# Performance work log

Hardware: AMD Instinct MI355X
Metric: run time of the kernel (lower is better)

## Reference

```python
import jax, jax.numpy as jnp
import numpy as np
from math import sqrt

BLOCK = 64  # block_size from init_kwargs


def setup_inputs() -> dict:
    key = jax.random.key(0)
    kq, kk, kv = jax.random.split(key, 3)
    b, t, e = 16, 8192, 64
    return {
        "Q": jax.random.normal(kq, (b, t, e), dtype=jnp.float32),
        "K": jax.random.normal(kk, (b, t, e), dtype=jnp.float32),
        "V": jax.random.normal(kv, (b, t, e), dtype=jnp.float32),
    }


def reference(Q, K, V):
    b, t, e = Q.shape
    # strided column indices: last position of every block
    cols = jnp.arange(BLOCK - 1, t, BLOCK)            # [n_cols] = [t // BLOCK]
    # scores of every query against the gathered key columns
    Z = jnp.einsum('bte,bce->btc', Q, K[:, cols]) / sqrt(e)  # [b, t, n_cols]
    # causal mask: query at position i may not attend to a column j > i
    causal = jnp.arange(t)[:, None] < cols[None, :]   # [t, n_cols], True = masked
    Z = jnp.where(causal, -jnp.inf, Z)
    # rows before the first column (i < BLOCK-1) are fully masked -> keep zeros
    A = jnp.zeros_like(Z).at[:, BLOCK - 1:].set(
        jax.nn.softmax(Z[:, BLOCK - 1:], axis=-1))
    out = jnp.einsum('btc,bce->bte', A, V[:, cols])   # [b, t, e]
    return out, A
```

## Files before the change

kernel.cpp:

```cpp
#include <hip/hip_runtime.h>
#include <math.h>


#define TSEQ 8192
#define EDIM 64
#define NCOL 128
#define NBATCH 16
#define MPG 4

typedef __attribute__((ext_vector_type(8))) short short8;
typedef __attribute__((ext_vector_type(4))) short short4v;
typedef __attribute__((ext_vector_type(4))) float f32x4;

__device__ __forceinline__ unsigned short f2bf(float f) {
    unsigned int u = __float_as_uint(f);
    return (unsigned short)((u + 0x7fffu + ((u >> 16) & 1u)) >> 16);
}

__global__ __launch_bounds__(256, 2)
void cba_kernel(const float* __restrict__ Q,
                const float* __restrict__ K,
                const float* __restrict__ V,
                float* __restrict__ Out,
                float* __restrict__ A)
{
    __shared__ unsigned short Kc[NCOL][72];
    __shared__ unsigned short VcT[EDIM][136];
    __shared__ unsigned short Aw[64][136];

    const int tid  = threadIdx.x;
    const int lane = tid & 63;
    const int wid  = tid >> 6;
    const int b    = blockIdx.x >> 5;
    const int mg   = blockIdx.x & 31;

    const int c   = lane & 15;
    const int g   = lane >> 4;
    const int kq  = g << 3;
    const int cb  = g << 2;
    const int r   = (wid << 4) + c;

    float4 qf[4];
    {
        const int m0 = mg * MPG;
        const float* qp = Q + ((size_t)b * TSEQ + (m0 << 6) + r) * EDIM;
        qf[0] = *(const float4*)(qp + kq);
        qf[1] = *(const float4*)(qp + kq + 4);
        qf[2] = *(const float4*)(qp + 32 + kq);
        qf[3] = *(const float4*)(qp + 32 + kq + 4);
    }

    {
        const int j = tid >> 1;
        const int h = (tid & 1) << 5;
        const size_t src = ((size_t)b * TSEQ + (j * 64 + 63)) * EDIM + h;
        const float4* ks = (const float4*)(K + src);
        const float4* vs = (const float4*)(V + src);
        #pragma unroll
        for (int t = 0; t < 8; ++t) {
            float4 kf = ks[t];
            unsigned int p0 = (unsigned int)f2bf(kf.x) | ((unsigned int)f2bf(kf.y) << 16);
            unsigned int p1 = (unsigned int)f2bf(kf.z) | ((unsigned int)f2bf(kf.w) << 16);
            *(unsigned int*)&Kc[j][h + 4 * t]     = p0;
            *(unsigned int*)&Kc[j][h + 4 * t + 2] = p1;
        }
        #pragma unroll
        for (int t = 0; t < 8; ++t) {
            float4 vf = vs[t];
            VcT[h + 4 * t + 0][j] = f2bf(vf.x);
            VcT[h + 4 * t + 1][j] = f2bf(vf.y);
            VcT[h + 4 * t + 2][j] = f2bf(vf.z);
            VcT[h + 4 * t + 3][j] = f2bf(vf.w);
        }
    }
    __syncthreads();

    for (int it = 0; it < MPG; ++it) {
        const int m = mg * MPG + it;
        const size_t rowbase = (size_t)b * TSEQ + ((size_t)m << 6);

        short8 qa[2];
        #pragma unroll
        for (int s = 0; s < 2; ++s) {
            float4 f0 = qf[2 * s], f1 = qf[2 * s + 1];
            short8 v;
            v[0] = (short)f2bf(f0.x * 0.125f); v[1] = (short)f2bf(f0.y * 0.125f);
            v[2] = (short)f2bf(f0.z * 0.125f); v[3] = (short)f2bf(f0.w * 0.125f);
            v[4] = (short)f2bf(f1.x * 0.125f); v[5] = (short)f2bf(f1.y * 0.125f);
            v[6] = (short)f2bf(f1.z * 0.125f); v[7] = (short)f2bf(f1.w * 0.125f);
            qa[s] = v;
        }

        f32x4 acc[8];
        #pragma unroll
        for (int t = 0; t < 8; ++t) acc[t] = (f32x4)0.f;
        #pragma unroll
        for (int t = 0; t < 8; ++t) {
            const unsigned short* kr = &Kc[(t << 4) + c][0];
            short8 b0 = *(const short8*)(kr + kq);
            short8 b1 = *(const short8*)(kr + 32 + kq);
            acc[t] = __builtin_amdgcn_mfma_f32_16x16x32_bf16(b0, qa[0], acc[t], 0, 0, 0);
            acc[t] = __builtin_amdgcn_mfma_f32_16x16x32_bf16(b1, qa[1], acc[t], 0, 0, 0);
        }

        if (it + 1 < MPG) {
            const float* qp = Q + (rowbase + 64 + r) * EDIM;
            qf[0] = *(const float4*)(qp + kq);
            qf[1] = *(const float4*)(qp + kq + 4);
            qf[2] = *(const float4*)(qp + 32 + kq);
            qf[3] = *(const float4*)(qp + 32 + kq + 4);
        }

        const int nv = m + (r == 63 ? 1 : 0);
        float sum = 0.f;
        #pragma unroll
        for (int t = 0; t < 8; ++t) {
            const int j0 = (t << 4) + cb;
            #pragma unroll
            for (int reg = 0; reg < 4; ++reg) {
                float e = (j0 + reg < nv) ? __expf(acc[t][reg]) : 0.f;
                acc[t][reg] = e;
                sum += e;
            }
        }
        sum += __shfl_xor(sum, 16);
        sum += __shfl_xor(sum, 32);
        const float rinv = (sum > 0.f) ? 1.0f / sum : 0.f;
        #pragma unroll
        for (int t = 0; t < 8; ++t) {
            acc[t][0] *= rinv; acc[t][1] *= rinv;
            acc[t][2] *= rinv; acc[t][3] *= rinv;
        }

        {
            float* ap = A + (rowbase + r) * NCOL + cb;
            #pragma unroll
            for (int t = 0; t < 8; ++t)
                *(f32x4*)(ap + (t << 4)) = acc[t];
        }

        asm volatile("" ::: "memory");
        #pragma unroll
        for (int t = 0; t < 8; ++t) {
            short4v w;
            w[0] = (short)f2bf(acc[t][0]); w[1] = (short)f2bf(acc[t][1]);
            w[2] = (short)f2bf(acc[t][2]); w[3] = (short)f2bf(acc[t][3]);
            *(short4v*)&Aw[r][(t << 4) + cb] = w;
        }
        asm volatile("s_waitcnt lgkmcnt(0)" ::: "memory");

        short8 af[4];
        {
            const unsigned short* ar = &Aw[r][0];
            #pragma unroll
            for (int s = 0; s < 4; ++s)
                af[s] = *(const short8*)(ar + (s << 5) + kq);
        }
        f32x4 oacc[4];
        #pragma unroll
        for (int te = 0; te < 4; ++te) oacc[te] = (f32x4)0.f;
        #pragma unroll
        for (int te = 0; te < 4; ++te) {
            const unsigned short* vr = &VcT[(te << 4) + c][0];
            #pragma unroll
            for (int s = 0; s < 4; ++s) {
                short8 va = *(const short8*)(vr + (s << 5) + kq);
                oacc[te] = __builtin_amdgcn_mfma_f32_16x16x32_bf16(va, af[s], oacc[te], 0, 0, 0);
            }
        }

        {
            float* op = Out + (rowbase + r) * EDIM + cb;
            #pragma unroll
            for (int te = 0; te < 4; ++te)
                *(f32x4*)(op + (te << 4)) = oacc[te];
        }
    }
}

extern "C" void kernel_launch(void* const* d_in, const int* in_sizes, int n_in,
                              void* d_out, int out_size, void* d_ws, size_t ws_size,
                              hipStream_t stream) {
    const float* Q = (const float*)d_in[0];
    const float* K = (const float*)d_in[1];
    const float* V = (const float*)d_in[2];
    float* Out = (float*)d_out;
    float* A   = Out + (size_t)NBATCH * TSEQ * EDIM;

    cba_kernel<<<dim3(NBATCH * 32), dim3(256), 0, stream>>>(Q, K, V, Out, A);
}
```

Before: 174.8 us.

## Replace LDS staging of attention weights with lane shuffles and double the grid

The softmax weights are now moved from the score accumulator layout into MFMA A-operand layout with cross-lane shuffles instead of a write and read through a shared-memory tile. Dropping that tile frees LDS, which allows 4 blocks per CU instead of 2. Each block now handles 2 row groups instead of 4, so the grid doubles to 1024 blocks. The cost is that the K/V column gather and bf16 conversion into shared memory run twice as often, and the shuffles add instructions of their own.

```diff
diff --git a/kernel.cpp b/kernel.cpp
--- a/kernel.cpp
+++ b/kernel.cpp
@@ -6,18 +6,20 @@
 #define EDIM 64
 #define NCOL 128
 #define NBATCH 16
-#define MPG 4
+#define MPG 2
 
 typedef __attribute__((ext_vector_type(8))) short short8;
-typedef __attribute__((ext_vector_type(4))) short short4v;
 typedef __attribute__((ext_vector_type(4))) float f32x4;
 
 __device__ __forceinline__ unsigned short f2bf(float f) {
     unsigned int u = __float_as_uint(f);
     return (unsigned short)((u + 0x7fffu + ((u >> 16) & 1u)) >> 16);
 }
+__device__ __forceinline__ unsigned int packbf(float a, float b) {
+    return (unsigned int)f2bf(a) | ((unsigned int)f2bf(b) << 16);
+}
 
-__global__ __launch_bounds__(256, 2)
+__global__ __launch_bounds__(256, 4)
 void cba_kernel(const float* __restrict__ Q,
                 const float* __restrict__ K,
                 const float* __restrict__ V,
@@ -26,13 +28,12 @@
 {
     __shared__ unsigned short Kc[NCOL][72];
     __shared__ unsigned short VcT[EDIM][136];
-    __shared__ unsigned short Aw[64][136];
 
     const int tid  = threadIdx.x;
     const int lane = tid & 63;
     const int wid  = tid >> 6;
-    const int b    = blockIdx.x >> 5;
-    const int mg   = blockIdx.x & 31;
+    const int b    = blockIdx.x >> 6;
+    const int mg   = blockIdx.x & 63;
 
     const int c   = lane & 15;
     const int g   = lane >> 4;
@@ -59,10 +60,8 @@
         #pragma unroll
         for (int t = 0; t < 8; ++t) {
             float4 kf = ks[t];
-            unsigned int p0 = (unsigned int)f2bf(kf.x) | ((unsigned int)f2bf(kf.y) << 16);
-            unsigned int p1 = (unsigned int)f2bf(kf.z) | ((unsigned int)f2bf(kf.w) << 16);
-            *(unsigned int*)&Kc[j][h + 4 * t]     = p0;
-            *(unsigned int*)&Kc[j][h + 4 * t + 2] = p1;
+            *(unsigned int*)&Kc[j][h + 4 * t]     = packbf(kf.x, kf.y);
+            *(unsigned int*)&Kc[j][h + 4 * t + 2] = packbf(kf.z, kf.w);
         }
         #pragma unroll
         for (int t = 0; t < 8; ++t) {
@@ -74,6 +73,10 @@
         }
     }
     __syncthreads();
+
+    const int srcA  = c + ((((g << 1)    ) & 3) << 4);
+    const int srcB  = c + ((((g << 1) + 1) & 3) << 4);
+    const bool hiSel = (lane & 32) != 0;
 
     for (int it = 0; it < MPG; ++it) {
         const int m = mg * MPG + it;
@@ -139,23 +142,27 @@
                 *(f32x4*)(ap + (t << 4)) = acc[t];
         }
 
-        asm volatile("" ::: "memory");
+        unsigned int w[16];
         #pragma unroll
         for (int t = 0; t < 8; ++t) {
-            short4v w;
-            w[0] = (short)f2bf(acc[t][0]); w[1] = (short)f2bf(acc[t][1]);
-            w[2] = (short)f2bf(acc[t][2]); w[3] = (short)f2bf(acc[t][3]);
-            *(short4v*)&Aw[r][(t << 4) + cb] = w;
+            w[2 * t]     = packbf(acc[t][0], acc[t][1]);
+            w[2 * t + 1] = packbf(acc[t][2], acc[t][3]);
         }
-        asm volatile("s_waitcnt lgkmcnt(0)" ::: "memory");
 
         short8 af[4];
-        {
-            const unsigned short* ar = &Aw[r][0];
+        #pragma unroll
+        for (int s = 0; s < 4; ++s) {
+            union { unsigned int d[4]; short8 v; } u;
             #pragma unroll
-            for (int s = 0; s < 4; ++s)
-                af[s] = *(const short8*)(ar + (s << 5) + kq);
+            for (int jd = 0; jd < 4; ++jd) {
+                const int src = (jd < 2) ? srcA : srcB;
+                unsigned int lo = __shfl(w[(s << 2) + (jd & 1)],     src);
+                unsigned int hi = __shfl(w[(s << 2) + 2 + (jd & 1)], src);
+                u.d[jd] = hiSel ? hi : lo;
+            }
+            af[s] = u.v;
         }
+
         f32x4 oacc[4];
         #pragma unroll
         for (int te = 0; te < 4; ++te) oacc[te] = (f32x4)0.f;
@@ -187,5 +194,5 @@
     float* Out = (float*)d_out;
     float* A   = Out + (size_t)NBATCH * TSEQ * EDIM;
 
-    cba_kernel<<<dim3(NBATCH * 32), dim3(256), 0, stream>>>(Q, K, V, Out, A);
+    cba_kernel<<<dim3(NBATCH * 64), dim3(256), 0, stream>>>(Q, K, V, Out, A);
 }
```

After: 177.6 us. About the same (+1.6%).
